# Kernel tuning notes

Measured on AMD Instinct MI355X. Metric: run time of the kernel, lower is better.

Reference implementation:

```python
import jax, jax.numpy as jnp
import numpy as np

N_NODES = 50000
N_EDGES = 800000
D = 128
N_LAYERS = 5  # 1 input + 3 hidden + 1 output MaxAggConv layers


def setup_inputs() -> dict:
    key = jax.random.key(0)
    k1, k2, k3, k4 = jax.random.split(key, 4)
    x = jax.random.normal(k1, (N_NODES, D), dtype=jnp.float32)
    edge_index = jax.random.randint(k2, (2, N_EDGES), 0, N_NODES, dtype=jnp.int64)
    # Linear params per layer (all layers are D->D here): W [out,in], b [out]
    Ws = jax.random.normal(k3, (N_LAYERS, D, D), dtype=jnp.float32) * (1.0 / np.sqrt(D))
    bs = jax.random.normal(k4, (N_LAYERS, D), dtype=jnp.float32) * 0.01
    return {"x": x, "edge_index": edge_index, "Ws": Ws, "bs": bs}


def _max_agg_conv(x, src, dst, W, b, n_nodes):
    # Linear: x @ W^T + b  (nn.Linear convention)
    h = jnp.einsum('nd,od->no', x, W) + b
    # gather per-edge messages x_j (source nodes), scatter-max into targets
    m = jax.ops.segment_max(h[src], dst, num_segments=n_nodes)
    # PyG scatter-max fills nodes with no incoming edges with 0
    return jnp.where(jnp.isneginf(m), 0.0, m)


def reference(x, edge_index, Ws, bs):
    src = edge_index[0]
    dst = edge_index[1]
    n = x.shape[0]
    for i in range(N_LAYERS - 1):
        x = _max_agg_conv(x, src, dst, Ws[i], bs[i], n)
        x = jax.nn.silu(x)
    x = _max_agg_conv(x, src, dst, Ws[N_LAYERS - 1], bs[N_LAYERS - 1], n)
    return x
```

## Files before the change

### kernel.cpp

```cpp
#include <hip/hip_runtime.h>
#include <hip/hip_bf16.h>
#include <hip/hip_fp16.h>
#include <math.h>

#define DF 128
#define NLAYERS 5

typedef __attribute__((ext_vector_type(8))) _Float16 f16x8;
typedef __attribute__((ext_vector_type(4))) _Float16 f16x4;
typedef __attribute__((ext_vector_type(4))) float f32x4;

__device__ inline unsigned pkmax(unsigned a, unsigned b) {
    unsigned d;
    asm("v_pk_max_f16 %0, %1, %2" : "=v"(d) : "v"(a), "v"(b));
    return d;
}
__device__ inline float h2f(unsigned short u) {
    __half_raw r; r.x = u;
    return __half2float(__half(r));
}
__device__ inline float silu(float v) {
    return v * (1.0f / (1.0f + __expf(-v)));
}

__device__ inline void split8f(const float* p, f16x8& hi, f16x8& lo) {
    float4 v0 = *reinterpret_cast<const float4*>(p);
    float4 v1 = *reinterpret_cast<const float4*>(p + 4);
    float f[8] = {v0.x, v0.y, v0.z, v0.w, v1.x, v1.y, v1.z, v1.w};
#pragma unroll
    for (int j = 0; j < 8; ++j) {
        _Float16 a = (_Float16)f[j];
        hi[j] = a;
        lo[j] = (_Float16)(f[j] - (float)a);
    }
}


__global__ __launch_bounds__(256) void zero_kernel(int* __restrict__ p, int n) {
    int i = blockIdx.x * 256 + threadIdx.x;
    if (i < n) p[i] = 0;
}


__global__ __launch_bounds__(256) void prep_kernel(const int* __restrict__ dst,
        int* __restrict__ cnt, unsigned short* __restrict__ rank, int E, int nbE,
        const float* __restrict__ Ws, _Float16* __restrict__ whf,
        _Float16* __restrict__ wlf, int wt4) {
    int b = blockIdx.x;
    int t = threadIdx.x;
    if (b < nbE) {
        int i = b * 256 + t;
        if (i < E) rank[i] = (unsigned short)atomicAdd(&cnt[dst[i]], 1);
    } else {
        int i = (b - nbE) * 256 + t;
        if (i < wt4) {
            float4 v = reinterpret_cast<const float4*>(Ws)[i];
            float f[4] = {v.x, v.y, v.z, v.w};
            f16x4 h, l;
#pragma unroll
            for (int j = 0; j < 4; ++j) {
                _Float16 a = (_Float16)f[j];
                h[j] = a;
                l[j] = (_Float16)(f[j] - (float)a);
            }
            reinterpret_cast<f16x4*>(whf)[i] = h;
            reinterpret_cast<f16x4*>(wlf)[i] = l;
        }
    }
}


__global__ __launch_bounds__(256) void partial_sum_kernel(const int* __restrict__ cnt,
        int* __restrict__ bsum, int n) {
    __shared__ int red[256];
    int t = threadIdx.x;
    int i = blockIdx.x * 256 + t;
    red[t] = (i < n) ? cnt[i] : 0;
    __syncthreads();
    for (int d = 128; d > 0; d >>= 1) {
        if (t < d) red[t] += red[t + d];
        __syncthreads();
    }
    if (t == 0) bsum[blockIdx.x] = red[0];
}

__global__ __launch_bounds__(256) void scan_scatter_kernel(const int* __restrict__ cnt,
        const int* __restrict__ bsum, int* __restrict__ off, int n, int E, int nb) {
    __shared__ int sb[256];
    __shared__ int s[256];
    int t = threadIdx.x;
    int bv = (t < nb) ? bsum[t] : 0;
    sb[t] = bv;
    __syncthreads();
    for (int d = 1; d < 256; d <<= 1) {
        int u = (t >= d) ? sb[t - d] : 0;
        __syncthreads();
        sb[t] += u;
        __syncthreads();
    }
    int base = (blockIdx.x > 0) ? sb[blockIdx.x - 1] : 0;
    int i = blockIdx.x * 256 + t;
    int v = (i < n) ? cnt[i] : 0;
    s[t] = v;
    __syncthreads();
    for (int d = 1; d < 256; d <<= 1) {
        int u = (t >= d) ? s[t - d] : 0;
        __syncthreads();
        s[t] += u;
        __syncthreads();
    }
    int excl = s[t] - v + base;
    if (i < n) off[i] = excl;
    if (blockIdx.x == 0 && t == 0) off[n] = E;
}


__global__ __launch_bounds__(256, 3) void fill_gemm0_kernel(
        const int* __restrict__ src, const int* __restrict__ dst,
        const int* __restrict__ off, const unsigned short* __restrict__ rank,
        unsigned short* __restrict__ csr, int E, int nbE,
        const float* __restrict__ x,
        const _Float16* __restrict__ whf, const _Float16* __restrict__ wlf,
        const float* __restrict__ bias, __half* __restrict__ h, int n) {
    if (blockIdx.x < nbE) {
        int i = blockIdx.x * 256 + threadIdx.x;
        if (i < E) csr[off[dst[i]] + (int)rank[i]] = (unsigned short)src[i];
        return;
    }
    int bid = blockIdx.x - nbE;

    int wave = threadIdx.x >> 6;
    int lane = threadIdx.x & 63;
    int wm = wave >> 1;
    int wn = wave & 1;
    int m0 = bid * 64 + wm * 32;
    int n0 = wn * 64;
    int lr = lane & 15;
    int lk = lane >> 4;

    f32x4 acc[2][4];
#pragma unroll
    for (int mt = 0; mt < 2; ++mt)
#pragma unroll
        for (int nt = 0; nt < 4; ++nt) {
            float bv = bias[n0 + nt * 16 + lr];
            acc[mt][nt] = (f32x4){bv, bv, bv, bv};
        }

    int rowA0 = min(m0 + lr, n - 1);
    int rowA1 = min(m0 + 16 + lr, n - 1);

#pragma unroll
    for (int ks = 0; ks < 4; ++ks) {
        int ko = ks * 32 + lk * 8;
        f16x8 a0h, a0l, a1h, a1l;
        split8f(x + (size_t)rowA0 * DF + ko, a0h, a0l);
        split8f(x + (size_t)rowA1 * DF + ko, a1h, a1l);
#pragma unroll
        for (int nt = 0; nt < 4; ++nt) {
            int ncol = n0 + nt * 16 + lr;
            f16x8 wh = *(const f16x8*)(whf + ncol * DF + ko);
            f16x8 wl = *(const f16x8*)(wlf + ncol * DF + ko);
            acc[0][nt] = __builtin_amdgcn_mfma_f32_16x16x32_f16(a0h, wh, acc[0][nt], 0, 0, 0);
            acc[0][nt] = __builtin_amdgcn_mfma_f32_16x16x32_f16(a0l, wh, acc[0][nt], 0, 0, 0);
            acc[0][nt] = __builtin_amdgcn_mfma_f32_16x16x32_f16(a0h, wl, acc[0][nt], 0, 0, 0);
            acc[1][nt] = __builtin_amdgcn_mfma_f32_16x16x32_f16(a1h, wh, acc[1][nt], 0, 0, 0);
            acc[1][nt] = __builtin_amdgcn_mfma_f32_16x16x32_f16(a1l, wh, acc[1][nt], 0, 0, 0);
            acc[1][nt] = __builtin_amdgcn_mfma_f32_16x16x32_f16(a1h, wl, acc[1][nt], 0, 0, 0);
        }
    }

#pragma unroll
    for (int mt = 0; mt < 2; ++mt) {
        int rbase = m0 + mt * 16 + lk * 4;
#pragma unroll
        for (int j = 0; j < 4; ++j) {
            int r = rbase + j;
            if (r < n) {
#pragma unroll
                for (int nt = 0; nt < 4; ++nt)
                    h[(size_t)r * DF + n0 + nt * 16 + lr] = __float2half(acc[mt][nt][j]);
            }
        }
    }
}


__global__ __launch_bounds__(256, 3) void gemm_f16_kernel(
        const _Float16* __restrict__ xf,
        const _Float16* __restrict__ whf, const _Float16* __restrict__ wlf,
        const float* __restrict__ bias, __half* __restrict__ h, int n) {
    int wave = threadIdx.x >> 6;
    int lane = threadIdx.x & 63;
    int wm = wave >> 1;
    int wn = wave & 1;
    int m0 = blockIdx.x * 64 + wm * 32;
    int n0 = wn * 64;
    int lr = lane & 15;
    int lk = lane >> 4;

    f32x4 acc[2][4];
#pragma unroll
    for (int mt = 0; mt < 2; ++mt)
#pragma unroll
        for (int nt = 0; nt < 4; ++nt) {
            float bv = bias[n0 + nt * 16 + lr];
            acc[mt][nt] = (f32x4){bv, bv, bv, bv};
        }

    int rowA0 = min(m0 + lr, n - 1);
    int rowA1 = min(m0 + 16 + lr, n - 1);

#pragma unroll
    for (int ks = 0; ks < 4; ++ks) {
        int ko = ks * 32 + lk * 8;
        f16x8 a0 = *(const f16x8*)(xf + (size_t)rowA0 * DF + ko);
        f16x8 a1 = *(const f16x8*)(xf + (size_t)rowA1 * DF + ko);
#pragma unroll
        for (int nt = 0; nt < 4; ++nt) {
            int ncol = n0 + nt * 16 + lr;
            f16x8 wh = *(const f16x8*)(whf + ncol * DF + ko);
            f16x8 wl = *(const f16x8*)(wlf + ncol * DF + ko);
            acc[0][nt] = __builtin_amdgcn_mfma_f32_16x16x32_f16(a0, wh, acc[0][nt], 0, 0, 0);
            acc[0][nt] = __builtin_amdgcn_mfma_f32_16x16x32_f16(a0, wl, acc[0][nt], 0, 0, 0);
            acc[1][nt] = __builtin_amdgcn_mfma_f32_16x16x32_f16(a1, wh, acc[1][nt], 0, 0, 0);
            acc[1][nt] = __builtin_amdgcn_mfma_f32_16x16x32_f16(a1, wl, acc[1][nt], 0, 0, 0);
        }
    }

#pragma unroll
    for (int mt = 0; mt < 2; ++mt) {
        int rbase = m0 + mt * 16 + lk * 4;
#pragma unroll
        for (int j = 0; j < 4; ++j) {
            int r = rbase + j;
            if (r < n) {
#pragma unroll
                for (int nt = 0; nt < 4; ++nt)
                    h[(size_t)r * DF + n0 + nt * 16 + lr] = __float2half(acc[mt][nt][j]);
            }
        }
    }
}


__global__ __launch_bounds__(256) void agg_kernel(const __half* __restrict__ hin,
        const int* __restrict__ off, const unsigned short* __restrict__ csr,
        float* __restrict__ out, _Float16* __restrict__ xf, int n, int split) {
    int wid = threadIdx.x >> 6;
    int lane = threadIdx.x & 63;
    int pair = blockIdx.x * 4 + wid;
    int nodeA = pair * 2;
    if (nodeA >= n) return;
    int nodeB = nodeA + 1;
    bool hasB = (nodeB < n);

    int q = lane >> 4;
    int c = lane & 15;

    int begA = off[nodeA], endA = off[nodeA + 1];
    int begB = hasB ? off[nodeB] : 0;
    int endB = hasB ? off[nodeB + 1] : 0;
    int degA = endA - begA, degB = endB - begB;
    int e1A = endA - 1, e1B = endB - 1;

    unsigned a0 = 0xFC00FC00u, a1 = a0, a2 = a0, a3 = a0;
    unsigned b0 = a0, b1 = a0, b2 = a0, b3 = a0;

    int nch = max((degA + 63) >> 6, (degB + 63) >> 6);
    for (int ch = 0; ch < nch; ++ch) {
        int baseo = ch << 6;
        bool doA = baseo < degA, doB = baseo < degB;
        int idA = 0, idB = 0;
        if (doA) idA = csr[min(begA + baseo + lane, e1A)];
        if (doB) idB = csr[min(begB + baseo + lane, e1B)];
        int limA = doA ? min(degA - baseo, 64) : 0;
        int limB = doB ? min(degB - baseo, 64) : 0;
        int lim = max(limA, limB);
        for (int t = 0; t < lim; t += 16) {
            if (t < limA) {
                int i0 = __shfl(idA, t + q);
                int i1 = __shfl(idA, t + q + 4);
                int i2 = __shfl(idA, t + q + 8);
                int i3 = __shfl(idA, t + q + 12);
                uint4 g0 = *(const uint4*)((const char*)hin + ((size_t)i0 << 8) + (c << 4));
                uint4 g1 = *(const uint4*)((const char*)hin + ((size_t)i1 << 8) + (c << 4));
                uint4 g2 = *(const uint4*)((const char*)hin + ((size_t)i2 << 8) + (c << 4));
                uint4 g3 = *(const uint4*)((const char*)hin + ((size_t)i3 << 8) + (c << 4));
                a0 = pkmax(a0, pkmax(pkmax(g0.x, g1.x), pkmax(g2.x, g3.x)));
                a1 = pkmax(a1, pkmax(pkmax(g0.y, g1.y), pkmax(g2.y, g3.y)));
                a2 = pkmax(a2, pkmax(pkmax(g0.z, g1.z), pkmax(g2.z, g3.z)));
                a3 = pkmax(a3, pkmax(pkmax(g0.w, g1.w), pkmax(g2.w, g3.w)));
            }
            if (t < limB) {
                int i0 = __shfl(idB, t + q);
                int i1 = __shfl(idB, t + q + 4);
                int i2 = __shfl(idB, t + q + 8);
                int i3 = __shfl(idB, t + q + 12);
                uint4 g0 = *(const uint4*)((const char*)hin + ((size_t)i0 << 8) + (c << 4));
                uint4 g1 = *(const uint4*)((const char*)hin + ((size_t)i1 << 8) + (c << 4));
                uint4 g2 = *(const uint4*)((const char*)hin + ((size_t)i2 << 8) + (c << 4));
                uint4 g3 = *(const uint4*)((const char*)hin + ((size_t)i3 << 8) + (c << 4));
                b0 = pkmax(b0, pkmax(pkmax(g0.x, g1.x), pkmax(g2.x, g3.x)));
                b1 = pkmax(b1, pkmax(pkmax(g0.y, g1.y), pkmax(g2.y, g3.y)));
                b2 = pkmax(b2, pkmax(pkmax(g0.z, g1.z), pkmax(g2.z, g3.z)));
                b3 = pkmax(b3, pkmax(pkmax(g0.w, g1.w), pkmax(g2.w, g3.w)));
            }
        }
    }

    a0 = pkmax(a0, (unsigned)__shfl_xor((int)a0, 16));
    a0 = pkmax(a0, (unsigned)__shfl_xor((int)a0, 32));
    a1 = pkmax(a1, (unsigned)__shfl_xor((int)a1, 16));
    a1 = pkmax(a1, (unsigned)__shfl_xor((int)a1, 32));
    a2 = pkmax(a2, (unsigned)__shfl_xor((int)a2, 16));
    a2 = pkmax(a2, (unsigned)__shfl_xor((int)a2, 32));
    a3 = pkmax(a3, (unsigned)__shfl_xor((int)a3, 16));
    a3 = pkmax(a3, (unsigned)__shfl_xor((int)a3, 32));
    b0 = pkmax(b0, (unsigned)__shfl_xor((int)b0, 16));
    b0 = pkmax(b0, (unsigned)__shfl_xor((int)b0, 32));
    b1 = pkmax(b1, (unsigned)__shfl_xor((int)b1, 16));
    b1 = pkmax(b1, (unsigned)__shfl_xor((int)b1, 32));
    b2 = pkmax(b2, (unsigned)__shfl_xor((int)b2, 16));
    b2 = pkmax(b2, (unsigned)__shfl_xor((int)b2, 32));
    b3 = pkmax(b3, (unsigned)__shfl_xor((int)b3, 16));
    b3 = pkmax(b3, (unsigned)__shfl_xor((int)b3, 32));

    int myNode; unsigned r0, r1, r2, r3; bool empty;
    if (q == 0) {
        myNode = nodeA; r0 = a0; r1 = a1; r2 = a2; r3 = a3; empty = (degA == 0);
    } else if (q == 1 && hasB) {
        myNode = nodeB; r0 = b0; r1 = b1; r2 = b2; r3 = b3; empty = (degB == 0);
    } else {
        return;
    }

    float f[8];
    f[0] = h2f((unsigned short)(r0 & 0xFFFF)); f[1] = h2f((unsigned short)(r0 >> 16));
    f[2] = h2f((unsigned short)(r1 & 0xFFFF)); f[3] = h2f((unsigned short)(r1 >> 16));
    f[4] = h2f((unsigned short)(r2 & 0xFFFF)); f[5] = h2f((unsigned short)(r2 >> 16));
    f[6] = h2f((unsigned short)(r3 & 0xFFFF)); f[7] = h2f((unsigned short)(r3 >> 16));
    if (empty) {
#pragma unroll
        for (int j = 0; j < 8; ++j) f[j] = 0.0f;
    }

    if (split) {
        f16x8 v;
#pragma unroll
        for (int j = 0; j < 8; ++j) v[j] = (_Float16)silu(f[j]);
        *reinterpret_cast<f16x8*>(xf + (size_t)myNode * DF + c * 8) = v;
    } else {
        float4* o = (float4*)(out + (size_t)myNode * DF + c * 8);
        o[0] = make_float4(f[0], f[1], f[2], f[3]);
        o[1] = make_float4(f[4], f[5], f[6], f[7]);
    }
}


extern "C" void kernel_launch(void* const* d_in, const int* in_sizes, int n_in,
                              void* d_out, int out_size, void* d_ws, size_t ws_size,
                              hipStream_t stream) {
    const float* x  = (const float*)d_in[0];
    const int*   ei = (const int*)d_in[1];
    const float* Ws = (const float*)d_in[2];
    const float* bs = (const float*)d_in[3];
    float* out = (float*)d_out;

    int N = in_sizes[0] / DF;
    int E = in_sizes[1] / 2;
    const int* src = ei;
    const int* dst = ei + E;

    char* w = (char*)d_ws;
    auto carve = [&](size_t bytes) {
        char* p = w;
        w += (bytes + 255) & ~(size_t)255;
        return p;
    };
    int nb = (N + 255) / 256;
    int*            cnt  = (int*)carve((size_t)(N + 1) * sizeof(int));
    int*            off  = (int*)carve((size_t)(N + 1) * sizeof(int));
    int*            bsum = (int*)carve((size_t)nb * sizeof(int));
    unsigned short* rank = (unsigned short*)carve((size_t)E * sizeof(unsigned short));
    unsigned short* csr  = (unsigned short*)carve((size_t)E * sizeof(unsigned short));
    __half*         h    = (__half*)carve((size_t)N * DF * sizeof(__half));
    _Float16*       xf   = (_Float16*)carve((size_t)N * DF * sizeof(_Float16));
    _Float16*       whf  = (_Float16*)carve((size_t)NLAYERS * DF * DF * sizeof(_Float16));
    _Float16*       wlf  = (_Float16*)carve((size_t)NLAYERS * DF * DF * sizeof(_Float16));

    int nbE = (E + 255) / 256;
    int wt4 = NLAYERS * DF * DF / 4;
    int nbW = (wt4 + 255) / 256;
    int ggrid = (N + 63) / 64;
    int agrid = (N + 7) / 8;

    zero_kernel<<<nb, 256, 0, stream>>>(cnt, N);
    prep_kernel<<<nbE + nbW, 256, 0, stream>>>(dst, cnt, rank, E, nbE, Ws, whf, wlf, wt4);
    partial_sum_kernel<<<nb, 256, 0, stream>>>(cnt, bsum, N);
    scan_scatter_kernel<<<nb, 256, 0, stream>>>(cnt, bsum, off, N, E, nb);

    fill_gemm0_kernel<<<nbE + ggrid, 256, 0, stream>>>(
        src, dst, off, rank, csr, E, nbE, x, whf, wlf, bs, h, N);

    for (int layer = 1; layer < NLAYERS; ++layer) {
        agg_kernel<<<agrid, 256, 0, stream>>>(h, off, csr, out, xf, N, 1);
        const _Float16* whl = whf + (size_t)layer * DF * DF;
        const _Float16* wll = wlf + (size_t)layer * DF * DF;
        const float* bl = bs + (size_t)layer * DF;
        gemm_f16_kernel<<<ggrid, 256, 0, stream>>>(xf, whl, wll, bl, h, N);
    }
    agg_kernel<<<agrid, 256, 0, stream>>>(h, off, csr, out, NULL, N, 0);
}
```

Baseline: 325.6 us.

## Split aggregation feature dimension across four blocks, one edge per lane group

The aggregation kernel now splits the 128-wide feature row into four 32-channel quarters, each handled by a separate block. Lane groups of four cover one edge at a time, so a wave gathers 16 edges per step instead of 4 edges with 4 loads each. The grid grows fourfold, and block indices are interleaved so neighbouring blocks share node groups and can reuse CSR and offset data in cache. In exchange, every block reloads the offsets and CSR indices and does the shuffles for only a quarter of the features, and each gather is now 64 contiguous bytes rather than a full 256-byte row, which may hurt memory coalescing.

```diff
diff --git a/kernel.cpp b/kernel.cpp
--- a/kernel.cpp
+++ b/kernel.cpp
@@ -249,14 +249,17 @@
         float* __restrict__ out, _Float16* __restrict__ xf, int n, int split) {
     int wid = threadIdx.x >> 6;
     int lane = threadIdx.x & 63;
-    int pair = blockIdx.x * 4 + wid;
-    int nodeA = pair * 2;
+    int bid = blockIdx.x;
+    int q = (bid & 7) >> 1;
+    int idx = ((bid >> 3) << 1) | (bid & 1);
+    int nodeA = idx * 8 + wid * 2;
     if (nodeA >= n) return;
     int nodeB = nodeA + 1;
     bool hasB = (nodeB < n);
 
-    int q = lane >> 4;
-    int c = lane & 15;
+    int r = lane >> 2;
+    int c2 = lane & 3;
+    int qb = q * 64 + c2 * 16;
 
     int begA = off[nodeA], endA = off[nodeA + 1];
     int begB = hasB ? off[nodeB] : 0;
@@ -279,57 +282,36 @@
         int lim = max(limA, limB);
         for (int t = 0; t < lim; t += 16) {
             if (t < limA) {
-                int i0 = __shfl(idA, t + q);
-                int i1 = __shfl(idA, t + q + 4);
-                int i2 = __shfl(idA, t + q + 8);
-                int i3 = __shfl(idA, t + q + 12);
-                uint4 g0 = *(const uint4*)((const char*)hin + ((size_t)i0 << 8) + (c << 4));
-                uint4 g1 = *(const uint4*)((const char*)hin + ((size_t)i1 << 8) + (c << 4));
-                uint4 g2 = *(const uint4*)((const char*)hin + ((size_t)i2 << 8) + (c << 4));
-                uint4 g3 = *(const uint4*)((const char*)hin + ((size_t)i3 << 8) + (c << 4));
-                a0 = pkmax(a0, pkmax(pkmax(g0.x, g1.x), pkmax(g2.x, g3.x)));
-                a1 = pkmax(a1, pkmax(pkmax(g0.y, g1.y), pkmax(g2.y, g3.y)));
-                a2 = pkmax(a2, pkmax(pkmax(g0.z, g1.z), pkmax(g2.z, g3.z)));
-                a3 = pkmax(a3, pkmax(pkmax(g0.w, g1.w), pkmax(g2.w, g3.w)));
+                int i0 = __shfl(idA, t + r);
+                uint4 g = *(const uint4*)((const char*)hin + ((size_t)i0 << 8) + qb);
+                a0 = pkmax(a0, g.x); a1 = pkmax(a1, g.y);
+                a2 = pkmax(a2, g.z); a3 = pkmax(a3, g.w);
             }
             if (t < limB) {
-                int i0 = __shfl(idB, t + q);
-                int i1 = __shfl(idB, t + q + 4);
-                int i2 = __shfl(idB, t + q + 8);
-                int i3 = __shfl(idB, t + q + 12);
-                uint4 g0 = *(const uint4*)((const char*)hin + ((size_t)i0 << 8) + (c << 4));
-                uint4 g1 = *(const uint4*)((const char*)hin + ((size_t)i1 << 8) + (c << 4));
-                uint4 g2 = *(const uint4*)((const char*)hin + ((size_t)i2 << 8) + (c << 4));
-                uint4 g3 = *(const uint4*)((const char*)hin + ((size_t)i3 << 8) + (c << 4));
-                b0 = pkmax(b0, pkmax(pkmax(g0.x, g1.x), pkmax(g2.x, g3.x)));
-                b1 = pkmax(b1, pkmax(pkmax(g0.y, g1.y), pkmax(g2.y, g3.y)));
-                b2 = pkmax(b2, pkmax(pkmax(g0.z, g1.z), pkmax(g2.z, g3.z)));
-                b3 = pkmax(b3, pkmax(pkmax(g0.w, g1.w), pkmax(g2.w, g3.w)));
-            }
-        }
-    }
-
-    a0 = pkmax(a0, (unsigned)__shfl_xor((int)a0, 16));
-    a0 = pkmax(a0, (unsigned)__shfl_xor((int)a0, 32));
-    a1 = pkmax(a1, (unsigned)__shfl_xor((int)a1, 16));
-    a1 = pkmax(a1, (unsigned)__shfl_xor((int)a1, 32));
-    a2 = pkmax(a2, (unsigned)__shfl_xor((int)a2, 16));
-    a2 = pkmax(a2, (unsigned)__shfl_xor((int)a2, 32));
-    a3 = pkmax(a3, (unsigned)__shfl_xor((int)a3, 16));
-    a3 = pkmax(a3, (unsigned)__shfl_xor((int)a3, 32));
-    b0 = pkmax(b0, (unsigned)__shfl_xor((int)b0, 16));
-    b0 = pkmax(b0, (unsigned)__shfl_xor((int)b0, 32));
-    b1 = pkmax(b1, (unsigned)__shfl_xor((int)b1, 16));
-    b1 = pkmax(b1, (unsigned)__shfl_xor((int)b1, 32));
-    b2 = pkmax(b2, (unsigned)__shfl_xor((int)b2, 16));
-    b2 = pkmax(b2, (unsigned)__shfl_xor((int)b2, 32));
-    b3 = pkmax(b3, (unsigned)__shfl_xor((int)b3, 16));
-    b3 = pkmax(b3, (unsigned)__shfl_xor((int)b3, 32));
+                int i0 = __shfl(idB, t + r);
+                uint4 g = *(const uint4*)((const char*)hin + ((size_t)i0 << 8) + qb);
+                b0 = pkmax(b0, g.x); b1 = pkmax(b1, g.y);
+                b2 = pkmax(b2, g.z); b3 = pkmax(b3, g.w);
+            }
+        }
+    }
+
+#pragma unroll
+    for (int d = 4; d <= 32; d <<= 1) {
+        a0 = pkmax(a0, (unsigned)__shfl_xor((int)a0, d));
+        a1 = pkmax(a1, (unsigned)__shfl_xor((int)a1, d));
+        a2 = pkmax(a2, (unsigned)__shfl_xor((int)a2, d));
+        a3 = pkmax(a3, (unsigned)__shfl_xor((int)a3, d));
+        b0 = pkmax(b0, (unsigned)__shfl_xor((int)b0, d));
+        b1 = pkmax(b1, (unsigned)__shfl_xor((int)b1, d));
+        b2 = pkmax(b2, (unsigned)__shfl_xor((int)b2, d));
+        b3 = pkmax(b3, (unsigned)__shfl_xor((int)b3, d));
+    }
 
     int myNode; unsigned r0, r1, r2, r3; bool empty;
-    if (q == 0) {
+    if (r == 0) {
         myNode = nodeA; r0 = a0; r1 = a1; r2 = a2; r3 = a3; empty = (degA == 0);
-    } else if (q == 1 && hasB) {
+    } else if (r == 1 && hasB) {
         myNode = nodeB; r0 = b0; r1 = b1; r2 = b2; r3 = b3; empty = (degB == 0);
     } else {
         return;
@@ -349,9 +331,9 @@
         f16x8 v;
 #pragma unroll
         for (int j = 0; j < 8; ++j) v[j] = (_Float16)silu(f[j]);
-        *reinterpret_cast<f16x8*>(xf + (size_t)myNode * DF + c * 8) = v;
+        *reinterpret_cast<f16x8*>(xf + (size_t)myNode * DF + q * 32 + c2 * 8) = v;
     } else {
-        float4* o = (float4*)(out + (size_t)myNode * DF + c * 8);
+        float4* o = (float4*)(out + (size_t)myNode * DF + q * 32 + c2 * 8);
         o[0] = make_float4(f[0], f[1], f[2], f[3]);
         o[1] = make_float4(f[4], f[5], f[6], f[7]);
     }
@@ -393,7 +375,8 @@
     int wt4 = NLAYERS * DF * DF / 4;
     int nbW = (wt4 + 255) / 256;
     int ggrid = (N + 63) / 64;
-    int agrid = (N + 7) / 8;
+    int ngrp = (N + 7) / 8;
+    int agrid = 8 * ((ngrp + 1) / 2);
 
     zero_kernel<<<nb, 256, 0, stream>>>(cnt, N);
     prep_kernel<<<nbE + nbW, 256, 0, stream>>>(dst, cnt, rank, E, nbE, Ws, whf, wlf, wt4);
```

Result: slower. 475.5 us (+46.0%).
